# Performance work log

Hardware: AMD Instinct MI355X
Metric: run time of the kernel (lower is better)

The kernel has to match this reference:

```python
import jax, jax.numpy as jnp
import numpy as np

B, Cin, Cout, H, W = 32, 16, 16, 64, 64
S = 2                      # shuffle_scale
K = 3                      # neighbors == conv kernel == stride
C1 = (Cin + 2) * S * S     # 72 channels after coord-concat + pixel_unshuffle
N = (H // S) * (W // S)    # 1024 tokens
EPS = 1e-12


def setup_inputs() -> dict:
    key = jax.random.key(0)
    ks = jax.random.split(key, 5)
    x = jax.random.normal(ks[0], (B, Cin, H, W), jnp.float32)
    # value projection over token dim: nn.Linear(num_tokens, num_tokens)
    Wv = jax.random.normal(ks[1], (N, N), jnp.float32) / np.sqrt(N).astype(np.float32)
    bv = jnp.zeros((N,), jnp.float32)
    # Conv1d(C1 -> C1, kernel=K, stride=K)
    conv_w = jax.random.normal(ks[2], (C1, C1, K), jnp.float32) / np.sqrt(C1 * K).astype(np.float32)
    conv_b = jnp.zeros((C1,), jnp.float32)
    # pointwise Conv2d(out_channels+2 -> out_channels, 1x1)
    pw_w = jax.random.normal(ks[3], (Cout, Cin + 2), jnp.float32) / np.sqrt(Cin + 2).astype(np.float32)
    pw_b = jnp.zeros((Cout,), jnp.float32)
    return dict(x=x, Wv=Wv, bv=bv, conv_w=conv_w, conv_b=conv_b, pw_w=pw_w, pw_b=pw_b)


def _coords(b, h, w):
    # torch meshgrid(indexing='ij') then F.normalize(p=2, dim=1) per pixel
    xg = jnp.broadcast_to(jnp.arange(h, dtype=jnp.float32)[:, None], (h, w))
    yg = jnp.broadcast_to(jnp.arange(w, dtype=jnp.float32)[None, :], (h, w))
    xy = jnp.stack([xg, yg], axis=0)                      # [2,H,W]
    nrm = jnp.maximum(jnp.linalg.norm(xy, axis=0, keepdims=True), EPS)
    xy = xy / nrm
    return jnp.broadcast_to(xy[None], (b, 2, h, w))


def _pixel_unshuffle(t, s):
    b, c, h, w = t.shape
    t = t.reshape(b, c, h // s, s, w // s, s)
    return t.transpose(0, 1, 3, 5, 2, 4).reshape(b, c * s * s, h // s, w // s)


def _pixel_shuffle(t, s):
    b, c, h, w = t.shape
    t = t.reshape(b, c // (s * s), s, s, h, w)
    return t.transpose(0, 1, 4, 2, 5, 3).reshape(b, c // (s * s), h * s, w * s)


def reference(x, Wv, bv, conv_w, conv_b, pw_w, pw_b):
    b = x.shape[0]
    # coord-concat -> pixel_unshuffle -> flatten
    xc = jnp.concatenate([x, _coords(b, H, W)], axis=1)    # [B,18,64,64]
    xu = _pixel_unshuffle(xc, S)                           # [B,72,32,32]
    t = xu.reshape(b, C1, N)                               # [B,72,1024]
    # V projection along the token dimension
    v = jnp.einsum('bcn,mn->bcm', t, Wv) + bv              # [B,C1,N]
    # cosine similarity between tokens
    tn = t / jnp.maximum(jnp.linalg.norm(t, axis=1, keepdims=True), EPS)
    sim = jnp.einsum('bcn,bcm->bnm', tn, tn)               # [B,N,N]
    vals, idx = jax.lax.top_k(sim, K)                      # [B,N,K] (similarity: largest)
    attn = jax.nn.softmax(vals, axis=-1)                   # [B,N,K]
    # gather top-K neighbor values, weight by attention
    neigh = jnp.take_along_axis(v[:, :, None, :], idx[:, None, :, :], axis=3)  # [B,C1,N,K]
    prime = neigh * attn[:, None, :, :]                    # [B,C1,N,K]
    # Conv1d(kernel=K, stride=K) over the [B,C1,N*K] prime == einsum over k
    out1d = jnp.einsum('bcnk,ock->bon', prime, conv_w) + conv_b[None, :, None]  # [B,C1,N]
    # unflatten -> pixel_shuffle -> pointwise 1x1 conv
    xs = _pixel_shuffle(out1d.reshape(b, C1, H // S, W // S), S)  # [B,18,64,64]
    return jnp.einsum('bchw,oc->bohw', xs, pw_w) + pw_b[None, :, None, None]
```

## Files before the change

kernel.cpp:

```cpp
#include <hip/hip_runtime.h>
#include <math.h>

#define BB   32
#define CIN  16
#define C1   72
#define NTOK 1024
#define HH   64
#define WW2  64

typedef float f32x4 __attribute__((ext_vector_type(4)));
typedef short s16x8 __attribute__((ext_vector_type(8)));
typedef short s16x4 __attribute__((ext_vector_type(4)));

__device__ __forceinline__ unsigned short f2bf(float f) {
  unsigned int u = __float_as_uint(f);
  unsigned int r = (u + 0x7FFFu + ((u >> 16) & 1u)) >> 16;
  return (unsigned short)r;
}
__device__ __forceinline__ float bf2f(unsigned short s) {
  return __uint_as_float(((unsigned int)s) << 16);
}

__global__ __launch_bounds__(256) void k0_wcvt(const float* __restrict__ Wv,
                                               short* __restrict__ wh,
                                               short* __restrict__ wl) {
  int i4 = (blockIdx.x * 256 + threadIdx.x) * 4;
  float4 v = *(const float4*)&Wv[i4];
  unsigned short h0 = f2bf(v.x), h1 = f2bf(v.y), h2 = f2bf(v.z), h3 = f2bf(v.w);
  s16x4 hv = { (short)h0, (short)h1, (short)h2, (short)h3 };
  s16x4 lv = { (short)f2bf(v.x - bf2f(h0)), (short)f2bf(v.y - bf2f(h1)),
               (short)f2bf(v.z - bf2f(h2)), (short)f2bf(v.w - bf2f(h3)) };
  *(s16x4*)&wh[i4] = hv;
  *(s16x4*)&wl[i4] = lv;
}

__global__ __launch_bounds__(128) void k1_build(const float* __restrict__ x,
                                                short* __restrict__ th,
                                                short* __restrict__ tl,
                                                short* __restrict__ ts0,
                                                short* __restrict__ ts1,
                                                short* __restrict__ ts2) {
  int gid = blockIdx.x * 128 + threadIdx.x;
  int b = gid >> 10;
  int n = gid & 1023;
  int hh = n >> 5, ww = n & 31;
  float vals[C1];
  float ss = 0.f;
#pragma unroll
  for (int c1 = 0; c1 < C1; ++c1) {
    int c = c1 >> 2, sh = (c1 >> 1) & 1, sw = c1 & 1;
    int h = 2 * hh + sh, w = 2 * ww + sw;
    float val;
    if (c < CIN) {
      val = x[((b * CIN + c) * HH + h) * WW2 + w];
    } else {
      float r = fmaxf(sqrtf((float)(h * h + w * w)), 1e-12f);
      val = (c == CIN ? (float)h : (float)w) / r;
    }
    vals[c1] = val;
    ss += val * val;
  }
  float inv = 1.0f / fmaxf(sqrtf(ss), 1e-12f);
#pragma unroll
  for (int c1 = 0; c1 < C1; ++c1) {
    int o = (b * C1 + c1) * NTOK + n;
    unsigned short h = f2bf(vals[c1]);
    th[o] = (short)h;
    tl[o] = (short)f2bf(vals[c1] - bf2f(h));
  }
  int nt = n >> 4, nl = n & 15;
#pragma unroll
  for (int ks = 0; ks < 3; ++ks)
#pragma unroll
    for (int g = 0; g < 4; ++g) {
      s16x8 v0, v1, v2;
#pragma unroll
      for (int j = 0; j < 8; ++j) {
        int c = ks * 32 + g * 8 + j;
        float f = (c < C1) ? vals[c] * inv : 0.f;
        unsigned short h0 = f2bf(f);
        float r0 = f - bf2f(h0);
        unsigned short h1 = f2bf(r0);
        float r1 = r0 - bf2f(h1);
        unsigned short h2 = f2bf(r1);
        v0[j] = (short)h0; v1[j] = (short)h1; v2[j] = (short)h2;
      }
      int off = (((b * 3 + ks) * 64 + nt) * 64 + (g * 16 + nl)) * 8;
      *(s16x8*)(ts0 + off) = v0;
      *(s16x8*)(ts1 + off) = v1;
      *(s16x8*)(ts2 + off) = v2;
    }
}

#define K2S 32
__global__ __launch_bounds__(256) void k2_vproj(const short* __restrict__ th,
                                                const short* __restrict__ tl,
                                                const short* __restrict__ wh,
                                                const short* __restrict__ wl,
                                                const float* __restrict__ bv,
                                                float* __restrict__ v_t) {
  __shared__ short sA[2][2][2048];
  __shared__ short sB[2][2][2048];
  int wg = blockIdx.x;
  int xcd = wg & 7;
  int q = wg >> 3;
  int row0 = (q >> 1) * 64;
  int col0 = (xcd * 2 + (q & 1)) * 64;
  int tid = threadIdx.x;
  int wv = tid >> 6, lane = tid & 63;

  int srow = tid >> 2, skc = tid & 3;
  int slot = (((srow >> 4) * 64) + (srow & 15) + 16 * skc) * 8;
  const short* gAh = th + (row0 + srow) * 1024 + skc * 8;
  const short* gAl = tl + (row0 + srow) * 1024 + skc * 8;
  const short* gBh = wh + (col0 + srow) * 1024 + skc * 8;
  const short* gBl = wl + (col0 + srow) * 1024 + skc * 8;

  s16x8 pah = *(const s16x8*)gAh;
  s16x8 pal = *(const s16x8*)gAl;
  s16x8 pbh = *(const s16x8*)gBh;
  s16x8 pbl = *(const s16x8*)gBl;
  *(s16x8*)&sA[0][0][slot] = pah;  *(s16x8*)&sA[0][1][slot] = pal;
  *(s16x8*)&sB[0][0][slot] = pbh;  *(s16x8*)&sB[0][1][slot] = pbl;

  f32x4 acc0 = {0,0,0,0}, acc1 = {0,0,0,0}, acc2 = {0,0,0,0}, acc3 = {0,0,0,0};
  __syncthreads();

  int cur = 0;
#pragma unroll 1
  for (int ks = 0; ks < 32; ++ks) {
    if (ks < 31) {
      pah = *(const s16x8*)(gAh + (ks + 1) * K2S);
      pal = *(const s16x8*)(gAl + (ks + 1) * K2S);
      pbh = *(const s16x8*)(gBh + (ks + 1) * K2S);
      pbl = *(const s16x8*)(gBl + (ks + 1) * K2S);
    }
    s16x8 ah = *(const s16x8*)&sA[cur][0][(wv * 64 + lane) * 8];
    s16x8 al = *(const s16x8*)&sA[cur][1][(wv * 64 + lane) * 8];
#pragma unroll
    for (int ct = 0; ct < 4; ++ct) {
      s16x8 bh = *(const s16x8*)&sB[cur][0][(ct * 64 + lane) * 8];
      s16x8 bl = *(const s16x8*)&sB[cur][1][(ct * 64 + lane) * 8];
      f32x4& a = (ct == 0 ? acc0 : ct == 1 ? acc1 : ct == 2 ? acc2 : acc3);
      a = __builtin_amdgcn_mfma_f32_16x16x32_bf16(ah, bh, a, 0, 0, 0);
      a = __builtin_amdgcn_mfma_f32_16x16x32_bf16(ah, bl, a, 0, 0, 0);
      a = __builtin_amdgcn_mfma_f32_16x16x32_bf16(al, bh, a, 0, 0, 0);
    }
    if (ks < 31) {
      *(s16x8*)&sA[cur ^ 1][0][slot] = pah;
      *(s16x8*)&sA[cur ^ 1][1][slot] = pal;
      *(s16x8*)&sB[cur ^ 1][0][slot] = pbh;
      *(s16x8*)&sB[cur ^ 1][1][slot] = pbl;
    }
    __syncthreads();
    cur ^= 1;
  }

#pragma unroll
  for (int ct = 0; ct < 4; ++ct) {
    f32x4 a = (ct == 0 ? acc0 : ct == 1 ? acc1 : ct == 2 ? acc2 : acc3);
    int colg = col0 + ct * 16 + (lane & 15);
    float bias = bv[colg];
#pragma unroll
    for (int i = 0; i < 4; ++i) {
      int rowg = row0 + wv * 16 + (lane >> 4) * 4 + i;
      int bb = rowg / 72;
      int cc = rowg - bb * 72;
      v_t[(bb * NTOK + colg) * C1 + cc] = a[i] + bias;
    }
  }
}

#define INS(TV, TI, d, di)                                              \
  {                                                                     \
    if ((d) > TV[0] || ((d) == TV[0] && (di) < TI[0])) {                \
      TV[2] = TV[1]; TI[2] = TI[1];                                     \
      TV[1] = TV[0]; TI[1] = TI[0];                                     \
      TV[0] = (d);   TI[0] = (di);                                      \
    } else if ((d) > TV[1] || ((d) == TV[1] && (di) < TI[1])) {         \
      TV[2] = TV[1]; TI[2] = TI[1];                                     \
      TV[1] = (d);   TI[1] = (di);                                      \
    } else if ((d) > TV[2] || ((d) == TV[2] && (di) < TI[2])) {         \
      TV[2] = (d);   TI[2] = (di);                                      \
    }                                                                   \
  }

__global__ __launch_bounds__(256) void k3_topk(const short* __restrict__ ts0,
                                               const short* __restrict__ ts1,
                                               const short* __restrict__ ts2,
                                               int* __restrict__ idxo,
                                               float* __restrict__ attno) {
  __shared__ short btile[18432];
  int wg = blockIdx.x;
  int xcd = wg & 7;
  int q = wg >> 3;
  int b  = xcd * 4 + (q >> 3);
  int nb = q & 7;
  int tid = threadIdx.x;
  int wv = tid >> 6, lane = tid & 63;

  s16x8 Bf[2][3][3];
#pragma unroll
  for (int ns = 0; ns < 2; ++ns)
#pragma unroll
    for (int ks = 0; ks < 3; ++ks) {
      int nt = nb * 8 + wv * 2 + ns;
      int off = (((b * 3 + ks) * 64 + nt) * 64 + lane) * 8;
      Bf[ns][ks][0] = *(const s16x8*)(ts0 + off);
      Bf[ns][ks][1] = *(const s16x8*)(ts1 + off);
      Bf[ns][ks][2] = *(const s16x8*)(ts2 + off);
    }

  float tv0[3] = {-INFINITY, -INFINITY, -INFINITY};
  float tv1[3] = {-INFINITY, -INFINITY, -INFINITY};
  int   ti0[3] = {0x7fffffff, 0x7fffffff, 0x7fffffff};
  int   ti1[3] = {0x7fffffff, 0x7fffffff, 0x7fffffff};

#pragma unroll 1
  for (int ch = 0; ch < 16; ++ch) {
    int mt0 = ch * 4;
    __syncthreads();
#pragma unroll
    for (int lev = 0; lev < 3; ++lev) {
      const short* tsp = (lev == 0 ? ts0 : lev == 1 ? ts1 : ts2);
#pragma unroll
      for (int sub = 0; sub < 3; ++sub) {
        int r = tid + sub * 256;
        int ks = r >> 8, mtl = (r >> 6) & 3, ln = r & 63;
        int g = (((b * 3 + ks) * 64 + (mt0 + mtl)) * 64 + ln) * 8;
        *(s16x8*)&btile[(((ks * 3 + lev) * 4 + mtl) * 64 + ln) * 8] =
            *(const s16x8*)(tsp + g);
      }
    }
    __syncthreads();

#pragma unroll
    for (int mtl = 0; mtl < 4; ++mtl) {
      f32x4 acc0 = {0, 0, 0, 0}, acc1 = {0, 0, 0, 0};
#pragma unroll
      for (int ks = 0; ks < 3; ++ks) {
        s16x8 a0 = *(const s16x8*)&btile[(((ks * 3 + 0) * 4 + mtl) * 64 + lane) * 8];
        s16x8 a1 = *(const s16x8*)&btile[(((ks * 3 + 1) * 4 + mtl) * 64 + lane) * 8];
        s16x8 a2 = *(const s16x8*)&btile[(((ks * 3 + 2) * 4 + mtl) * 64 + lane) * 8];
        acc0 = __builtin_amdgcn_mfma_f32_16x16x32_bf16(a0, Bf[0][ks][0], acc0, 0, 0, 0);
        acc0 = __builtin_amdgcn_mfma_f32_16x16x32_bf16(a0, Bf[0][ks][1], acc0, 0, 0, 0);
        acc0 = __builtin_amdgcn_mfma_f32_16x16x32_bf16(a1, Bf[0][ks][0], acc0, 0, 0, 0);
        acc0 = __builtin_amdgcn_mfma_f32_16x16x32_bf16(a0, Bf[0][ks][2], acc0, 0, 0, 0);
        acc0 = __builtin_amdgcn_mfma_f32_16x16x32_bf16(a1, Bf[0][ks][1], acc0, 0, 0, 0);
        acc0 = __builtin_amdgcn_mfma_f32_16x16x32_bf16(a2, Bf[0][ks][0], acc0, 0, 0, 0);
        acc1 = __builtin_amdgcn_mfma_f32_16x16x32_bf16(a0, Bf[1][ks][0], acc1, 0, 0, 0);
        acc1 = __builtin_amdgcn_mfma_f32_16x16x32_bf16(a0, Bf[1][ks][1], acc1, 0, 0, 0);
        acc1 = __builtin_amdgcn_mfma_f32_16x16x32_bf16(a1, Bf[1][ks][0], acc1, 0, 0, 0);
        acc1 = __builtin_amdgcn_mfma_f32_16x16x32_bf16(a0, Bf[1][ks][2], acc1, 0, 0, 0);
        acc1 = __builtin_amdgcn_mfma_f32_16x16x32_bf16(a1, Bf[1][ks][1], acc1, 0, 0, 0);
        acc1 = __builtin_amdgcn_mfma_f32_16x16x32_bf16(a2, Bf[1][ks][0], acc1, 0, 0, 0);
      }
      int mb = ch * 64 + mtl * 16 + ((lane >> 4) << 2);
      float mx0 = fmaxf(fmaxf(acc0[0], acc0[1]), fmaxf(acc0[2], acc0[3]));
      if (mx0 > tv0[2]) {
        INS(tv0, ti0, acc0[0], mb + 0); INS(tv0, ti0, acc0[1], mb + 1);
        INS(tv0, ti0, acc0[2], mb + 2); INS(tv0, ti0, acc0[3], mb + 3);
      }
      float mx1 = fmaxf(fmaxf(acc1[0], acc1[1]), fmaxf(acc1[2], acc1[3]));
      if (mx1 > tv1[2]) {
        INS(tv1, ti1, acc1[0], mb + 0); INS(tv1, ti1, acc1[1], mb + 1);
        INS(tv1, ti1, acc1[2], mb + 2); INS(tv1, ti1, acc1[3], mb + 3);
      }
    }
  }

  __syncthreads();
  float* mv = (float*)btile;
  int*   mi = ((int*)btile) + 1536;
  int g2 = lane >> 4;
  {
    int nl0 = wv * 32 + (lane & 15);
#pragma unroll
    for (int j = 0; j < 3; ++j) {
      mv[((nl0)      * 4 + g2) * 3 + j] = tv0[j];
      mi[((nl0)      * 4 + g2) * 3 + j] = ti0[j];
      mv[((nl0 + 16) * 4 + g2) * 3 + j] = tv1[j];
      mi[((nl0 + 16) * 4 + g2) * 3 + j] = ti1[j];
    }
  }
  __syncthreads();
  if (tid < 128) {
    float fv[3] = {-INFINITY, -INFINITY, -INFINITY};
    int   fi[3] = {0x7fffffff, 0x7fffffff, 0x7fffffff};
#pragma unroll
    for (int g = 0; g < 4; ++g)
#pragma unroll
      for (int j = 0; j < 3; ++j) {
        float d  = mv[(tid * 4 + g) * 3 + j];
        int   di = mi[(tid * 4 + g) * 3 + j];
        INS(fv, fi, d, di);
      }
    float e1 = expf(fv[1] - fv[0]), e2 = expf(fv[2] - fv[0]);
    float inv = 1.0f / (1.0f + e1 + e2);
    int nn = nb * 128 + tid;
    int ob = (b * NTOK + nn) * 3;
    idxo[ob] = fi[0]; idxo[ob + 1] = fi[1]; idxo[ob + 2] = fi[2];
    attno[ob] = inv; attno[ob + 1] = e1 * inv; attno[ob + 2] = e2 * inv;
  }
}

__global__ __launch_bounds__(256) void k4_conv1d(const float* __restrict__ v_t,
                                                 const int* __restrict__ idx,
                                                 const float* __restrict__ attn,
                                                 const float* __restrict__ conv_w,
                                                 const float* __restrict__ conv_b,
                                                 float* __restrict__ out1d) {
  __shared__ float prime[64][220];
  __shared__ int   sidx[64][3];
  __shared__ float satt[64][3];
  int wg = blockIdx.x;
  int xcd = wg & 7;
  int q = wg >> 3;
  int b  = xcd * 4 + (q >> 4);
  int n0 = (q & 15) * 64;
  int tid = threadIdx.x;
  if (tid < 192) {
    int tok = tid / 3, k = tid % 3;
    sidx[tok][k] = idx[(b * NTOK + n0 + tok) * 3 + k];
    satt[tok][k] = attn[(b * NTOK + n0 + tok) * 3 + k];
  }
  __syncthreads();
  for (int u = tid; u < 64 * 3 * 18; u += 256) {
    int tok = u / 54;
    int r   = u - tok * 54;
    int k   = r / 18;
    int c4  = r - k * 18;
    float4 val = *(const float4*)&v_t[(b * NTOK + sidx[tok][k]) * C1 + c4 * 4];
    float s = satt[tok][k];
    int base = (c4 * 4) * 3 + k;
    prime[tok][base]     = val.x * s;
    prime[tok][base + 3] = val.y * s;
    prime[tok][base + 6] = val.z * s;
    prime[tok][base + 9] = val.w * s;
  }
  __syncthreads();
  int tok = tid & 63;
  int obase = __builtin_amdgcn_readfirstlane((int)(tid >> 6)) * 18;
  float acc[18];
#pragma unroll
  for (int j = 0; j < 18; ++j) acc[j] = 0.f;
  for (int ck4 = 0; ck4 < 54; ++ck4) {
    float4 p4 = *(const float4*)&prime[tok][ck4 * 4];
#pragma unroll
    for (int j = 0; j < 18; ++j) {
      float4 w4 = *(const float4*)&conv_w[(obase + j) * 216 + ck4 * 4];
      acc[j] += p4.x * w4.x + p4.y * w4.y + p4.z * w4.z + p4.w * w4.w;
    }
  }
#pragma unroll
  for (int j = 0; j < 18; ++j) {
    int o = obase + j;
    out1d[(b * C1 + o) * NTOK + n0 + tok] = acc[j] + conv_b[o];
  }
}

__global__ __launch_bounds__(256) void k5_pw(const float* __restrict__ out1d,
                                             const float* __restrict__ pw_w,
                                             const float* __restrict__ pw_b,
                                             float* __restrict__ out) {
  int gid = blockIdx.x * 256 + threadIdx.x;
  int b = gid >> 12;
  int p = gid & 4095;
  int h = p >> 6, w = p & 63;
  int hh = h >> 1, ww = w >> 1;
  int c1base = ((h & 1) << 1) | (w & 1);
  int n = hh * 32 + ww;
  float xs[18];
#pragma unroll
  for (int c = 0; c < 18; ++c)
    xs[c] = out1d[(b * C1 + c * 4 + c1base) * NTOK + n];
#pragma unroll
  for (int o = 0; o < 16; ++o) {
    float a = pw_b[o];
#pragma unroll
    for (int c = 0; c < 18; ++c) a += xs[c] * pw_w[o * 18 + c];
    out[((b * 16 + o) << 12) + p] = a;
  }
}

extern "C" void kernel_launch(void* const* d_in, const int* in_sizes, int n_in,
                              void* d_out, int out_size, void* d_ws, size_t ws_size,
                              hipStream_t stream) {
  (void)in_sizes; (void)n_in; (void)out_size; (void)ws_size;
  const float* x      = (const float*)d_in[0];
  const float* Wv     = (const float*)d_in[1];
  const float* bv     = (const float*)d_in[2];
  const float* conv_w = (const float*)d_in[3];
  const float* conv_b = (const float*)d_in[4];
  const float* pw_w   = (const float*)d_in[5];
  const float* pw_b   = (const float*)d_in[6];
  float* out = (float*)d_out;

  char* ws = (char*)d_ws;
  short* th    = (short*)(ws);
  short* tl    = (short*)(ws + 4718592);
  float* out1d = (float*)(ws);
  short* wh    = (short*)(ws + 9437184);
  short* wl    = (short*)(ws + 11534336);
  int*   idx   = (int*)  (ws + 9437184);
  float* attn  = (float*)(ws + 9830400);
  short* ts0   = (short*)(ws + 13631488);
  short* ts1   = (short*)(ws + 19922944);
  short* ts2   = (short*)(ws + 26214400);
  float* v_t   = (float*)(ws + 32505856);

  k1_build<<<dim3((BB * NTOK) / 128), 128, 0, stream>>>(x, th, tl, ts0, ts1, ts2);
  k0_wcvt <<<dim3(1024), 256, 0, stream>>>(Wv, wh, wl);
  k2_vproj<<<dim3(576), 256, 0, stream>>>(th, tl, wh, wl, bv, v_t);
  k3_topk <<<dim3(256), 256, 0, stream>>>(ts0, ts1, ts2, idx, attn);
  k4_conv1d<<<dim3(512), 256, 0, stream>>>(v_t, idx, attn, conv_w, conv_b, out1d);
  k5_pw   <<<dim3((BB * 4096) / 256), 256, 0, stream>>>(out1d, pw_w, pw_b, out);
}
```

Measured before the change: 301.4 us.

## Split top-k similarity scan across four token-range blocks and merge partials

The top-k kernel now launches four times as many workgroups. Each one scans only a quarter of the candidate tokens and writes its partial top-3 values and indices to workspace. A new small kernel merges the 12 partial candidates per token and computes the softmax attention weights. The goal is to raise occupancy: the previous 256-block launch gave roughly one workgroup per CU. The cost is an extra launch, an extra round trip of partial results through global memory, and B-fragments reloaded by more blocks.

```diff
diff --git a/kernel.cpp b/kernel.cpp
--- a/kernel.cpp
+++ b/kernel.cpp
@@ -188,14 +188,16 @@
 __global__ __launch_bounds__(256) void k3_topk(const short* __restrict__ ts0,
                                                const short* __restrict__ ts1,
                                                const short* __restrict__ ts2,
-                                               int* __restrict__ idxo,
-                                               float* __restrict__ attno) {
+                                               float* __restrict__ pv,
+                                               int* __restrict__ pi) {
   __shared__ short btile[18432];
   int wg = blockIdx.x;
   int xcd = wg & 7;
   int q = wg >> 3;
-  int b  = xcd * 4 + (q >> 3);
-  int nb = q & 7;
+  int b  = xcd * 4 + (q >> 5);
+  int rem = q & 31;
+  int nb = rem >> 2;
+  int mh = rem & 3;
   int tid = threadIdx.x;
   int wv = tid >> 6, lane = tid & 63;
 
@@ -217,7 +219,7 @@
   int   ti1[3] = {0x7fffffff, 0x7fffffff, 0x7fffffff};
 
 #pragma unroll 1
-  for (int ch = 0; ch < 16; ++ch) {
+  for (int ch = mh * 4; ch < mh * 4 + 4; ++ch) {
     int mt0 = ch * 4;
     __syncthreads();
 #pragma unroll
@@ -295,13 +297,31 @@
         int   di = mi[(tid * 4 + g) * 3 + j];
         INS(fv, fi, d, di);
       }
-    float e1 = expf(fv[1] - fv[0]), e2 = expf(fv[2] - fv[0]);
-    float inv = 1.0f / (1.0f + e1 + e2);
     int nn = nb * 128 + tid;
-    int ob = (b * NTOK + nn) * 3;
-    idxo[ob] = fi[0]; idxo[ob + 1] = fi[1]; idxo[ob + 2] = fi[2];
-    attno[ob] = inv; attno[ob + 1] = e1 * inv; attno[ob + 2] = e2 * inv;
-  }
+    int ob = ((b * NTOK + nn) * 4 + mh) * 3;
+#pragma unroll
+    for (int j = 0; j < 3; ++j) { pv[ob + j] = fv[j]; pi[ob + j] = fi[j]; }
+  }
+}
+
+__global__ __launch_bounds__(256) void k3m(const float* __restrict__ pv,
+                                           const int* __restrict__ pi,
+                                           int* __restrict__ idxo,
+                                           float* __restrict__ attno) {
+  int r = blockIdx.x * 256 + threadIdx.x;
+  float fv[3] = {-INFINITY, -INFINITY, -INFINITY};
+  int   fi[3] = {0x7fffffff, 0x7fffffff, 0x7fffffff};
+#pragma unroll
+  for (int u = 0; u < 12; ++u) {
+    float d  = pv[r * 12 + u];
+    int   di = pi[r * 12 + u];
+    INS(fv, fi, d, di);
+  }
+  float e1 = expf(fv[1] - fv[0]), e2 = expf(fv[2] - fv[0]);
+  float inv = 1.0f / (1.0f + e1 + e2);
+  int ob = r * 3;
+  idxo[ob] = fi[0]; idxo[ob + 1] = fi[1]; idxo[ob + 2] = fi[2];
+  attno[ob] = inv; attno[ob + 1] = e1 * inv; attno[ob + 2] = e2 * inv;
 }
 
 __global__ __launch_bounds__(256) void k4_conv1d(const float* __restrict__ v_t,
@@ -399,6 +419,8 @@
   char* ws = (char*)d_ws;
   short* th    = (short*)(ws);
   short* tl    = (short*)(ws + 4718592);
+  float* pv    = (float*)(ws);
+  int*   pi    = (int*)  (ws + 2097152);
   float* out1d = (float*)(ws);
   short* wh    = (short*)(ws + 9437184);
   short* wl    = (short*)(ws + 11534336);
@@ -412,7 +434,8 @@
   k1_build<<<dim3((BB * NTOK) / 128), 128, 0, stream>>>(x, th, tl, ts0, ts1, ts2);
   k0_wcvt <<<dim3(1024), 256, 0, stream>>>(Wv, wh, wl);
   k2_vproj<<<dim3(576), 256, 0, stream>>>(th, tl, wh, wl, bv, v_t);
-  k3_topk <<<dim3(256), 256, 0, stream>>>(ts0, ts1, ts2, idx, attn);
+  k3_topk <<<dim3(1024), 256, 0, stream>>>(ts0, ts1, ts2, pv, pi);
+  k3m     <<<dim3(128), 256, 0, stream>>>(pv, pi, idx, attn);
   k4_conv1d<<<dim3(512), 256, 0, stream>>>(v_t, idx, attn, conv_w, conv_b, out1d);
   k5_pw   <<<dim3((BB * 4096) / 256), 256, 0, stream>>>(out1d, pw_w, pw_b, out);
 }
```

Measured after the change: 258.5 us. 14.2% less time.
